# Kernel optimization log

Hardware: AMD Instinct MI355X
Metric: run time of the kernel (lower is better)

The kernel has to match this reference:

```python
import jax, jax.numpy as jnp
import numpy as np

B, C, H, W = 4, 256, 256, 256
N_BOX = 64          # rois per batch element
S = 7               # roi_feature_size[0]
ROI_SCALE = 0.25    # world -> feature-map coordinate scale
WORLD = H / ROI_SCALE  # world extent ~1024


def setup_inputs() -> dict:
    key = jax.random.key(0)
    k1, k2, k3, k4 = jax.random.split(key, 4)
    feats = jax.random.normal(k1, (B, C, H, W), dtype=jnp.float32)
    centers = jax.random.uniform(k2, (B, N_BOX, 2), minval=0.0, maxval=WORLD)
    wh = jax.random.uniform(k3, (B, N_BOX, 2), minval=32.0, maxval=256.0)
    theta = jax.random.uniform(k4, (B, N_BOX, 1), minval=0.0, maxval=2.0 * np.pi)
    rois = jnp.concatenate([centers, wh, theta], axis=-1).astype(jnp.float32)  # [B,N,5]
    return {"feats": feats, "rois": rois}


def _rotated_roi_align(feats, rois, out_size):
    # feats: [B,C,H,W]; rois: [B,N,5] = (cx,cy,w,h,theta) in feature-map coords
    b, c, h, w = feats.shape
    n = rois.shape[1]
    feats_t = jnp.transpose(feats, (0, 2, 3, 1))            # [B,H,W,C]
    r = rois.reshape(b * n, 5)
    bidx = jnp.repeat(jnp.arange(b), n)                     # [BN]
    cx, cy, bw, bh, th = r[:, 0], r[:, 1], r[:, 2], r[:, 3], r[:, 4]
    # sample-point offsets in box-local coords (cell centers)
    lin = (jnp.arange(out_size, dtype=jnp.float32) + 0.5) / out_size - 0.5  # [S]
    u = lin[None, None, :] * bw[:, None, None]              # cols  [BN,1,S]
    v = lin[None, :, None] * bh[:, None, None]              # rows  [BN,S,1]
    ct, st = jnp.cos(th)[:, None, None], jnp.sin(th)[:, None, None]
    x = cx[:, None, None] + u * ct - v * st                 # [BN,S,S]
    y = cy[:, None, None] + u * st + v * ct                 # [BN,S,S]
    # bilinear sampling with zero padding outside the map
    x0 = jnp.floor(x); y0 = jnp.floor(y)
    x1 = x0 + 1.0;     y1 = y0 + 1.0
    wx1 = x - x0; wx0 = 1.0 - wx1
    wy1 = y - y0; wy0 = 1.0 - wy1

    def gather(xi, yi):
        valid = (xi >= 0) & (xi <= w - 1) & (yi >= 0) & (yi <= h - 1)
        xc = jnp.clip(xi, 0, w - 1).astype(jnp.int32)
        yc = jnp.clip(yi, 0, h - 1).astype(jnp.int32)
        vals = feats_t[bidx[:, None, None], yc, xc]          # [BN,S,S,C]
        return vals * valid[..., None].astype(feats.dtype)

    out = (gather(x0, y0) * (wx0 * wy0)[..., None]
           + gather(x1, y0) * (wx1 * wy0)[..., None]
           + gather(x0, y1) * (wx0 * wy1)[..., None]
           + gather(x1, y1) * (wx1 * wy1)[..., None])       # [BN,S,S,C]
    return jnp.transpose(out, (0, 3, 1, 2))                 # [BN,C,S,S]


def reference(feats, rois):
    # scale all roi entries except the trailing angle
    srois = jnp.concatenate([rois[..., :-1] * ROI_SCALE, rois[..., -1:]], axis=-1)
    return _rotated_roi_align(feats, srois, S)              # cat over batch -> [B*N,C,S,S]
```

## Files before the change

### kernel.cpp

```cpp
#include <hip/hip_runtime.h>

#define BB 4
#define CC 256
#define HH 256
#define WW 256
#define N_BOX 64
#define SS 7
#define NPTS (SS * SS)
#define NROI (BB * N_BOX)
#define CG 64
#define NG (CC / CG)
#define ITEMS (CG * NPTS)
#define ROI_SCALE 0.25f

__global__ __launch_bounds__(256) void rotated_roi_align_kernel(
    const float* __restrict__ feats,
    const float* __restrict__ rois,
    float* __restrict__ out)
{
    __shared__ int   s_off[4][NPTS];
    __shared__ float s_w[4][NPTS];

    const int r   = blockIdx.x;
    const int cq  = blockIdx.y;
    const int b   = r >> 6;
    const int tid = threadIdx.x;

    if (tid < NPTS) {
        const float cx = rois[r * 5 + 0] * ROI_SCALE;
        const float cy = rois[r * 5 + 1] * ROI_SCALE;
        const float bw = rois[r * 5 + 2] * ROI_SCALE;
        const float bh = rois[r * 5 + 3] * ROI_SCALE;
        const float th = rois[r * 5 + 4];
        const float ct = cosf(th);
        const float st = sinf(th);

        const int py = tid / SS;
        const int px = tid - py * SS;
        const float lu = (px + 0.5f) / (float)SS - 0.5f;
        const float lv = (py + 0.5f) / (float)SS - 0.5f;
        const float u = lu * bw;
        const float v = lv * bh;
        const float x = cx + u * ct - v * st;
        const float y = cy + u * st + v * ct;

        const float x0f = floorf(x), y0f = floorf(y);
        const float x1f = x0f + 1.0f, y1f = y0f + 1.0f;
        const float wx1 = x - x0f, wx0 = 1.0f - wx1;
        const float wy1 = y - y0f, wy0 = 1.0f - wy1;

        const bool vx0 = (x0f >= 0.0f) && (x0f <= (float)(WW - 1));
        const bool vx1 = (x1f >= 0.0f) && (x1f <= (float)(WW - 1));
        const bool vy0 = (y0f >= 0.0f) && (y0f <= (float)(HH - 1));
        const bool vy1 = (y1f >= 0.0f) && (y1f <= (float)(HH - 1));

        const int x0c = min(max((int)x0f, 0), WW - 1);
        const int x1c = min(max((int)x1f, 0), WW - 1);
        const int y0c = min(max((int)y0f, 0), HH - 1);
        const int y1c = min(max((int)y1f, 0), HH - 1);

        s_off[0][tid] = y0c * WW + x0c;  s_w[0][tid] = (vx0 && vy0) ? wx0 * wy0 : 0.0f;
        s_off[1][tid] = y0c * WW + x1c;  s_w[1][tid] = (vx1 && vy0) ? wx1 * wy0 : 0.0f;
        s_off[2][tid] = y1c * WW + x0c;  s_w[2][tid] = (vx0 && vy1) ? wx0 * wy1 : 0.0f;
        s_off[3][tid] = y1c * WW + x1c;  s_w[3][tid] = (vx1 && vy1) ? wx1 * wy1 : 0.0f;
    }
    __syncthreads();

    const float* plane_base = feats + ((size_t)b * CC + (size_t)cq * CG) * (HH * WW);
    float* ob = out + (size_t)r * CC * NPTS + (size_t)cq * CG * NPTS;

    #pragma unroll 4
    for (int i = tid; i < ITEMS; i += 256) {
        const int cl = i / NPTS;
        const int p  = i - cl * NPTS;
        const float* plane = plane_base + (size_t)cl * (HH * WW);
        const float v0 = plane[s_off[0][p]];
        const float v1 = plane[s_off[1][p]];
        const float v2 = plane[s_off[2][p]];
        const float v3 = plane[s_off[3][p]];
        ob[i] = s_w[0][p] * v0 + s_w[1][p] * v1 + s_w[2][p] * v2 + s_w[3][p] * v3;
    }
}

extern "C" void kernel_launch(void* const* d_in, const int* in_sizes, int n_in,
                              void* d_out, int out_size, void* d_ws, size_t ws_size,
                              hipStream_t stream) {
    const float* feats = (const float*)d_in[0];
    const float* rois  = (const float*)d_in[1];
    float* out = (float*)d_out;

    dim3 grid(NROI, NG);
    rotated_roi_align_kernel<<<grid, 256, 0, stream>>>(feats, rois, out);
}
```

Before: 401.9 us.

## Transpose features to channels-last in workspace before a coalesced float4 gather

Adds a tiled shared-memory transpose that converts the NCHW feature map into NHWC in the workspace buffer on every call. A new gather kernel then reads four contiguous channels per float4 load at each bilinear corner, accumulates the result, and transposes it back through shared memory into the [roi, C, S, S] output. This replaces the old pattern where every sample was a scattered 4-byte load from a different channel plane. The cost is a full read and write of the 268 MB feature tensor each call. If the workspace is too small, the code falls back to the original kernel.

```diff
diff --git a/kernel.cpp b/kernel.cpp
--- a/kernel.cpp
+++ b/kernel.cpp
@@ -4,28 +4,61 @@
 #define CC 256
 #define HH 256
 #define WW 256
+#define HWV (HH * WW)
 #define N_BOX 64
 #define SS 7
 #define NPTS (SS * SS)
 #define NROI (BB * N_BOX)
-#define CG 64
-#define NG (CC / CG)
-#define ITEMS (CG * NPTS)
 #define ROI_SCALE 0.25f
 
-__global__ __launch_bounds__(256) void rotated_roi_align_kernel(
-    const float* __restrict__ feats,
-    const float* __restrict__ rois,
+__global__ __launch_bounds__(256) void transpose_kernel(
+    const float* __restrict__ in,
     float* __restrict__ out)
 {
-    __shared__ int   s_off[4][NPTS];
-    __shared__ float s_w[4][NPTS];
-
-    const int r   = blockIdx.x;
-    const int cq  = blockIdx.y;
-    const int b   = r >> 6;
+    __shared__ float tile[64 * 65];
+
+    const int hw0 = blockIdx.x * 64;
+    const int c0  = blockIdx.y * 64;
+    const int b   = blockIdx.z;
     const int tid = threadIdx.x;
 
+    {
+        const int jq = tid & 15;
+        const int ir = tid >> 4;
+        const float* inb = in + ((size_t)(b * CC + c0) << 16) + hw0;
+        #pragma unroll
+        for (int k = 0; k < 4; ++k) {
+            const int i = ir + 16 * k;
+            const float4 v = *(const float4*)(inb + ((size_t)i << 16) + jq * 4);
+            tile[(jq * 4 + 0) * 65 + i] = v.x;
+            tile[(jq * 4 + 1) * 65 + i] = v.y;
+            tile[(jq * 4 + 2) * 65 + i] = v.z;
+            tile[(jq * 4 + 3) * 65 + i] = v.w;
+        }
+    }
+    __syncthreads();
+
+    {
+        const int iq = tid & 15;
+        const int jr = tid >> 4;
+        float* outb = out + (((size_t)b << 16) + hw0) * CC + c0;
+        #pragma unroll
+        for (int k = 0; k < 4; ++k) {
+            const int j = jr + 16 * k;
+            float4 v;
+            v.x = tile[j * 65 + iq * 4 + 0];
+            v.y = tile[j * 65 + iq * 4 + 1];
+            v.z = tile[j * 65 + iq * 4 + 2];
+            v.w = tile[j * 65 + iq * 4 + 3];
+            *(float4*)(outb + (size_t)j * CC + iq * 4) = v;
+        }
+    }
+}
+
+__device__ __forceinline__ void precompute_points(
+    const float* __restrict__ rois, int r, int tid,
+    int s_off[4][NPTS], float s_w[4][NPTS])
+{
     if (tid < NPTS) {
         const float cx = rois[r * 5 + 0] * ROI_SCALE;
         const float cy = rois[r * 5 + 1] * ROI_SCALE;
@@ -64,16 +97,83 @@
         s_off[2][tid] = y1c * WW + x0c;  s_w[2][tid] = (vx0 && vy1) ? wx0 * wy1 : 0.0f;
         s_off[3][tid] = y1c * WW + x1c;  s_w[3][tid] = (vx1 && vy1) ? wx1 * wy1 : 0.0f;
     }
-    __syncthreads();
-
-    const float* plane_base = feats + ((size_t)b * CC + (size_t)cq * CG) * (HH * WW);
-    float* ob = out + (size_t)r * CC * NPTS + (size_t)cq * CG * NPTS;
+}
+
+#define CGP 64
+#define NG2 (CC / CGP)
+#define TSTRIDE 65
+
+__global__ __launch_bounds__(256) void gather_cl_kernel(
+    const float* __restrict__ ft,
+    const float* __restrict__ rois,
+    float* __restrict__ out)
+{
+    __shared__ int   s_off[4][NPTS];
+    __shared__ float s_w[4][NPTS];
+    __shared__ float t[NPTS * TSTRIDE];
+
+    const int r   = blockIdx.x;
+    const int cg  = blockIdx.y;
+    const int b   = r >> 6;
+    const int tid = threadIdx.x;
+
+    precompute_points(rois, r, tid, s_off, s_w);
+    __syncthreads();
+
+    const float* base = ft + ((size_t)b << 16) * CC + cg * CGP;
+
+    for (int w = tid; w < NPTS * (CGP / 4); w += 256) {
+        const int p  = w >> 4;
+        const int cq = w & 15;
+        float4 acc = make_float4(0.f, 0.f, 0.f, 0.f);
+        #pragma unroll
+        for (int k = 0; k < 4; ++k) {
+            const float4 v = *(const float4*)(base + (size_t)s_off[k][p] * CC + cq * 4);
+            const float wk = s_w[k][p];
+            acc.x += wk * v.x;
+            acc.y += wk * v.y;
+            acc.z += wk * v.z;
+            acc.w += wk * v.w;
+        }
+        t[p * TSTRIDE + cq * 4 + 0] = acc.x;
+        t[p * TSTRIDE + cq * 4 + 1] = acc.y;
+        t[p * TSTRIDE + cq * 4 + 2] = acc.z;
+        t[p * TSTRIDE + cq * 4 + 3] = acc.w;
+    }
+    __syncthreads();
+
+    float* ob = out + ((size_t)r * CC + (size_t)cg * CGP) * NPTS;
+    for (int j = tid; j < CGP * NPTS; j += 256) {
+        const int c = j / NPTS;
+        const int p = j - c * NPTS;
+        ob[j] = t[p * TSTRIDE + c];
+    }
+}
+
+__global__ __launch_bounds__(256) void rotated_roi_align_fallback(
+    const float* __restrict__ feats,
+    const float* __restrict__ rois,
+    float* __restrict__ out)
+{
+    __shared__ int   s_off[4][NPTS];
+    __shared__ float s_w[4][NPTS];
+
+    const int r   = blockIdx.x;
+    const int cq  = blockIdx.y;
+    const int b   = r >> 6;
+    const int tid = threadIdx.x;
+
+    precompute_points(rois, r, tid, s_off, s_w);
+    __syncthreads();
+
+    const float* plane_base = feats + ((size_t)b * CC + (size_t)cq * 64) * HWV;
+    float* ob = out + (size_t)r * CC * NPTS + (size_t)cq * 64 * NPTS;
 
     #pragma unroll 4
-    for (int i = tid; i < ITEMS; i += 256) {
+    for (int i = tid; i < 64 * NPTS; i += 256) {
         const int cl = i / NPTS;
         const int p  = i - cl * NPTS;
-        const float* plane = plane_base + (size_t)cl * (HH * WW);
+        const float* plane = plane_base + (size_t)cl * HWV;
         const float v0 = plane[s_off[0][p]];
         const float v1 = plane[s_off[1][p]];
         const float v2 = plane[s_off[2][p]];
@@ -89,6 +189,16 @@
     const float* rois  = (const float*)d_in[1];
     float* out = (float*)d_out;
 
-    dim3 grid(NROI, NG);
-    rotated_roi_align_kernel<<<grid, 256, 0, stream>>>(feats, rois, out);
-}
+    const size_t need = (size_t)BB * CC * HWV * sizeof(float);
+
+    if (ws_size >= need) {
+        float* feats_t = (float*)d_ws;
+        dim3 g1(HWV / 64, CC / 64, BB);
+        transpose_kernel<<<g1, 256, 0, stream>>>(feats, feats_t);
+        dim3 g2(NROI, NG2);
+        gather_cl_kernel<<<g2, 256, 0, stream>>>(feats_t, rois, out);
+    } else {
+        dim3 grid(NROI, 4);
+        rotated_roi_align_fallback<<<grid, 256, 0, stream>>>(feats, rois, out);
+    }
+}
```

Measured after the change: 411.7 us. +2.4%, slower.

## Split ROI coordinate precompute into separate kernel and halve channel group size

Applied to the files above, without the earlier changes.

Moves the per-ROI sample-offset and weight computation (including sin/cos) into a small precompute kernel that writes to workspace, so each gather block only loads the 196 offsets and weights instead of recomputing them. Channel groups shrink from 64 to 32, doubling the grid to spread the scattered loads over more blocks, and the gather loop is restructured with a fixed trip count plus tail and a higher occupancy hint. The cost is an extra kernel launch and a round trip through global memory for the precomputed tables.

```diff
diff --git a/kernel.cpp b/kernel.cpp
--- a/kernel.cpp
+++ b/kernel.cpp
@@ -4,81 +4,114 @@
 #define CC 256
 #define HH 256
 #define WW 256
+#define HWV (HH * WW)
 #define N_BOX 64
 #define SS 7
 #define NPTS (SS * SS)
 #define NROI (BB * N_BOX)
-#define CG 64
-#define NG (CC / CG)
-#define ITEMS (CG * NPTS)
 #define ROI_SCALE 0.25f
 
-__global__ __launch_bounds__(256) void rotated_roi_align_kernel(
+#define CG 32
+#define NGRP (CC / CG)
+#define ITEMS (CG * NPTS)
+#define PPR (4 * NPTS)
+
+__global__ __launch_bounds__(64) void precompute_kernel(
+    const float* __restrict__ rois,
+    int* __restrict__ offs,
+    float* __restrict__ wts)
+{
+    const int r = blockIdx.x;
+    const int tid = threadIdx.x;
+    if (tid >= NPTS) return;
+
+    const float cx = rois[r * 5 + 0] * ROI_SCALE;
+    const float cy = rois[r * 5 + 1] * ROI_SCALE;
+    const float bw = rois[r * 5 + 2] * ROI_SCALE;
+    const float bh = rois[r * 5 + 3] * ROI_SCALE;
+    const float th = rois[r * 5 + 4];
+    const float ct = cosf(th);
+    const float st = sinf(th);
+
+    const int py = tid / SS;
+    const int px = tid - py * SS;
+    const float lu = (px + 0.5f) / (float)SS - 0.5f;
+    const float lv = (py + 0.5f) / (float)SS - 0.5f;
+    const float u = lu * bw;
+    const float v = lv * bh;
+    const float x = cx + u * ct - v * st;
+    const float y = cy + u * st + v * ct;
+
+    const float x0f = floorf(x), y0f = floorf(y);
+    const float x1f = x0f + 1.0f, y1f = y0f + 1.0f;
+    const float wx1 = x - x0f, wx0 = 1.0f - wx1;
+    const float wy1 = y - y0f, wy0 = 1.0f - wy1;
+
+    const bool vx0 = (x0f >= 0.0f) && (x0f <= (float)(WW - 1));
+    const bool vx1 = (x1f >= 0.0f) && (x1f <= (float)(WW - 1));
+    const bool vy0 = (y0f >= 0.0f) && (y0f <= (float)(HH - 1));
+    const bool vy1 = (y1f >= 0.0f) && (y1f <= (float)(HH - 1));
+
+    const int x0c = min(max((int)x0f, 0), WW - 1);
+    const int x1c = min(max((int)x1f, 0), WW - 1);
+    const int y0c = min(max((int)y0f, 0), HH - 1);
+    const int y1c = min(max((int)y1f, 0), HH - 1);
+
+    int*   ro = offs + (size_t)r * PPR;
+    float* rw = wts  + (size_t)r * PPR;
+    ro[0 * NPTS + tid] = y0c * WW + x0c;  rw[0 * NPTS + tid] = (vx0 && vy0) ? wx0 * wy0 : 0.0f;
+    ro[1 * NPTS + tid] = y0c * WW + x1c;  rw[1 * NPTS + tid] = (vx1 && vy0) ? wx1 * wy0 : 0.0f;
+    ro[2 * NPTS + tid] = y1c * WW + x0c;  rw[2 * NPTS + tid] = (vx0 && vy1) ? wx0 * wy1 : 0.0f;
+    ro[3 * NPTS + tid] = y1c * WW + x1c;  rw[3 * NPTS + tid] = (vx1 && vy1) ? wx1 * wy1 : 0.0f;
+}
+
+__global__ __launch_bounds__(256, 8) void gather_kernel(
     const float* __restrict__ feats,
-    const float* __restrict__ rois,
+    const int* __restrict__ offs,
+    const float* __restrict__ wts,
     float* __restrict__ out)
 {
-    __shared__ int   s_off[4][NPTS];
-    __shared__ float s_w[4][NPTS];
+    __shared__ int   s_off[PPR];
+    __shared__ float s_w[PPR];
 
     const int r   = blockIdx.x;
-    const int cq  = blockIdx.y;
+    const int cg  = blockIdx.y;
     const int b   = r >> 6;
     const int tid = threadIdx.x;
 
-    if (tid < NPTS) {
-        const float cx = rois[r * 5 + 0] * ROI_SCALE;
-        const float cy = rois[r * 5 + 1] * ROI_SCALE;
-        const float bw = rois[r * 5 + 2] * ROI_SCALE;
-        const float bh = rois[r * 5 + 3] * ROI_SCALE;
-        const float th = rois[r * 5 + 4];
-        const float ct = cosf(th);
-        const float st = sinf(th);
-
-        const int py = tid / SS;
-        const int px = tid - py * SS;
-        const float lu = (px + 0.5f) / (float)SS - 0.5f;
-        const float lv = (py + 0.5f) / (float)SS - 0.5f;
-        const float u = lu * bw;
-        const float v = lv * bh;
-        const float x = cx + u * ct - v * st;
-        const float y = cy + u * st + v * ct;
-
-        const float x0f = floorf(x), y0f = floorf(y);
-        const float x1f = x0f + 1.0f, y1f = y0f + 1.0f;
-        const float wx1 = x - x0f, wx0 = 1.0f - wx1;
-        const float wy1 = y - y0f, wy0 = 1.0f - wy1;
-
-        const bool vx0 = (x0f >= 0.0f) && (x0f <= (float)(WW - 1));
-        const bool vx1 = (x1f >= 0.0f) && (x1f <= (float)(WW - 1));
-        const bool vy0 = (y0f >= 0.0f) && (y0f <= (float)(HH - 1));
-        const bool vy1 = (y1f >= 0.0f) && (y1f <= (float)(HH - 1));
-
-        const int x0c = min(max((int)x0f, 0), WW - 1);
-        const int x1c = min(max((int)x1f, 0), WW - 1);
-        const int y0c = min(max((int)y0f, 0), HH - 1);
-        const int y1c = min(max((int)y1f, 0), HH - 1);
-
-        s_off[0][tid] = y0c * WW + x0c;  s_w[0][tid] = (vx0 && vy0) ? wx0 * wy0 : 0.0f;
-        s_off[1][tid] = y0c * WW + x1c;  s_w[1][tid] = (vx1 && vy0) ? wx1 * wy0 : 0.0f;
-        s_off[2][tid] = y1c * WW + x0c;  s_w[2][tid] = (vx0 && vy1) ? wx0 * wy1 : 0.0f;
-        s_off[3][tid] = y1c * WW + x1c;  s_w[3][tid] = (vx1 && vy1) ? wx1 * wy1 : 0.0f;
+    if (tid < PPR) {
+        s_off[tid] = offs[(size_t)r * PPR + tid];
+        s_w[tid]   = wts [(size_t)r * PPR + tid];
     }
     __syncthreads();
 
-    const float* plane_base = feats + ((size_t)b * CC + (size_t)cq * CG) * (HH * WW);
-    float* ob = out + (size_t)r * CC * NPTS + (size_t)cq * CG * NPTS;
+    const float* plane_base = feats + ((size_t)b * CC + (size_t)cg * CG) * HWV;
+    float* ob = out + ((size_t)r * CC + (size_t)cg * CG) * NPTS;
 
-    #pragma unroll 4
-    for (int i = tid; i < ITEMS; i += 256) {
+    #pragma unroll 3
+    for (int it = 0; it < 6; ++it) {
+        const int i  = tid + it * 256;
         const int cl = i / NPTS;
         const int p  = i - cl * NPTS;
-        const float* plane = plane_base + (size_t)cl * (HH * WW);
-        const float v0 = plane[s_off[0][p]];
-        const float v1 = plane[s_off[1][p]];
-        const float v2 = plane[s_off[2][p]];
-        const float v3 = plane[s_off[3][p]];
-        ob[i] = s_w[0][p] * v0 + s_w[1][p] * v1 + s_w[2][p] * v2 + s_w[3][p] * v3;
+        const float* plane = plane_base + (size_t)cl * HWV;
+        const float v0 = plane[s_off[0 * NPTS + p]];
+        const float v1 = plane[s_off[1 * NPTS + p]];
+        const float v2 = plane[s_off[2 * NPTS + p]];
+        const float v3 = plane[s_off[3 * NPTS + p]];
+        ob[i] = s_w[0 * NPTS + p] * v0 + s_w[1 * NPTS + p] * v1
+              + s_w[2 * NPTS + p] * v2 + s_w[3 * NPTS + p] * v3;
+    }
+    if (tid < ITEMS - 6 * 256) {
+        const int i  = tid + 6 * 256;
+        const int cl = i / NPTS;
+        const int p  = i - cl * NPTS;
+        const float* plane = plane_base + (size_t)cl * HWV;
+        const float v0 = plane[s_off[0 * NPTS + p]];
+        const float v1 = plane[s_off[1 * NPTS + p]];
+        const float v2 = plane[s_off[2 * NPTS + p]];
+        const float v3 = plane[s_off[3 * NPTS + p]];
+        ob[i] = s_w[0 * NPTS + p] * v0 + s_w[1 * NPTS + p] * v1
+              + s_w[2 * NPTS + p] * v2 + s_w[3 * NPTS + p] * v3;
     }
 }
 
@@ -89,6 +122,11 @@
     const float* rois  = (const float*)d_in[1];
     float* out = (float*)d_out;
 
-    dim3 grid(NROI, NG);
-    rotated_roi_align_kernel<<<grid, 256, 0, stream>>>(feats, rois, out);
+    int*   offs = (int*)d_ws;
+    float* wts  = (float*)((char*)d_ws + (size_t)NROI * PPR * sizeof(int));
+
+    precompute_kernel<<<NROI, 64, 0, stream>>>(rois, offs, wts);
+
+    dim3 g(NROI, NGRP);
+    gather_kernel<<<g, 256, 0, stream>>>(feats, offs, wts, out);
 }
```

After: 416.0 us. 3.5% more time.

## Precompute deduplicated float4 quad addresses and gather via shared memory

Applied to the files above, without the earlier changes.

Adds a precompute kernel that computes bilinear weights and deduplicates 16-byte-aligned quad addresses per ROI, storing slot indices in workspace. The gather kernel then loads each unique float4 quad once per channel into shared memory and combines the four taps from there, with 32 channels per block. This aims to cut redundant scattered global loads, but it serializes channels with two barriers per iteration, adds a second launch, and leaves most threads idle during combination.

```diff
diff --git a/kernel.cpp b/kernel.cpp
--- a/kernel.cpp
+++ b/kernel.cpp
@@ -4,26 +4,38 @@
 #define CC 256
 #define HH 256
 #define WW 256
+#define HWV (HH * WW)
 #define N_BOX 64
 #define SS 7
 #define NPTS (SS * SS)
 #define NROI (BB * N_BOX)
-#define CG 64
-#define NG (CC / CG)
-#define ITEMS (CG * NPTS)
 #define ROI_SCALE 0.25f
 
-__global__ __launch_bounds__(256) void rotated_roi_align_kernel(
-    const float* __restrict__ feats,
+#define NCAND (NPTS * 4)
+#define CG 32
+#define NGRP (CC / CG)
+
+#define WS_WTS_OFF   0
+#define WS_SLOT_OFF  (WS_WTS_OFF + NROI * NPTS * 16)
+#define WS_UOFF_OFF  (WS_SLOT_OFF + NROI * NPTS * 8)
+#define WS_APK_OFF   (WS_UOFF_OFF + NROI * NCAND * 4)
+#define WS_NU_OFF    (WS_APK_OFF + NROI * NPTS * 4)
+#define WS_NEED      (WS_NU_OFF + NROI * 4)
+
+__global__ __launch_bounds__(256) void precompute_kernel(
     const float* __restrict__ rois,
-    float* __restrict__ out)
+    float4* __restrict__ g_wts,
+    short4* __restrict__ g_slots,
+    int* __restrict__ g_uoff,
+    int* __restrict__ g_apk,
+    int* __restrict__ g_nu)
 {
-    __shared__ int   s_off[4][NPTS];
-    __shared__ float s_w[4][NPTS];
-
-    const int r   = blockIdx.x;
-    const int cq  = blockIdx.y;
-    const int b   = r >> 6;
+    __shared__ int cand[NCAND];
+    __shared__ int lead[NCAND];
+    __shared__ int flag[NCAND];
+    __shared__ int pre[NCAND];
+
+    const int r = blockIdx.x;
     const int tid = threadIdx.x;
 
     if (tid < NPTS) {
@@ -59,6 +71,151 @@
         const int y0c = min(max((int)y0f, 0), HH - 1);
         const int y1c = min(max((int)y1f, 0), HH - 1);
 
+        const int q0 = x0c & ~3;
+        const int q1 = x1c & ~3;
+        cand[tid * 4 + 0] = (y0c << 8) + q0;
+        cand[tid * 4 + 1] = (y0c << 8) + q1;
+        cand[tid * 4 + 2] = (y1c << 8) + q0;
+        cand[tid * 4 + 3] = (y1c << 8) + q1;
+
+        float4 w;
+        w.x = (vx0 && vy0) ? wx0 * wy0 : 0.0f;
+        w.y = (vx1 && vy0) ? wx1 * wy0 : 0.0f;
+        w.z = (vx0 && vy1) ? wx0 * wy1 : 0.0f;
+        w.w = (vx1 && vy1) ? wx1 * wy1 : 0.0f;
+        g_wts[(size_t)r * NPTS + tid] = w;
+        g_apk[(size_t)r * NPTS + tid] = (x0c & 3) | ((x1c & 3) << 2);
+    }
+    __syncthreads();
+
+    if (tid < NCAND) {
+        const int c = cand[tid];
+        int ld = tid;
+        for (int j = 0; j < NCAND; ++j) {
+            const int cj = cand[j];
+            if (j < tid && cj == c && ld == tid) ld = j;
+        }
+        lead[tid] = ld;
+        flag[tid] = (ld == tid) ? 1 : 0;
+    }
+    __syncthreads();
+
+    if (tid < NCAND) {
+        int s = 0;
+        for (int j = 0; j < NCAND; ++j) {
+            const int f = flag[j];
+            if (j < tid) s += f;
+        }
+        pre[tid] = s;
+        if (flag[tid]) g_uoff[(size_t)r * NCAND + s] = cand[tid];
+    }
+    __syncthreads();
+
+    if (tid < NPTS) {
+        short4 sl;
+        sl.x = (short)pre[lead[tid * 4 + 0]];
+        sl.y = (short)pre[lead[tid * 4 + 1]];
+        sl.z = (short)pre[lead[tid * 4 + 2]];
+        sl.w = (short)pre[lead[tid * 4 + 3]];
+        g_slots[(size_t)r * NPTS + tid] = sl;
+    }
+    if (tid == 0) g_nu[r] = pre[NCAND - 1] + flag[NCAND - 1];
+}
+
+__global__ __launch_bounds__(256, 8) void gather_kernel(
+    const float* __restrict__ feats,
+    const float4* __restrict__ g_wts,
+    const short4* __restrict__ g_slots,
+    const int* __restrict__ g_uoff,
+    const int* __restrict__ g_apk,
+    const int* __restrict__ g_nu,
+    float* __restrict__ out)
+{
+    __shared__ int    s_uoff[NCAND];
+    __shared__ short4 s_slot[NPTS];
+    __shared__ int    s_apk[NPTS];
+    __shared__ float4 s_wts[NPTS];
+    __shared__ float4 s_quad[NCAND];
+    __shared__ float  s_out[CG * NPTS];
+
+    const int r   = blockIdx.x;
+    const int cg  = blockIdx.y;
+    const int b   = r >> 6;
+    const int tid = threadIdx.x;
+
+    const int nu = g_nu[r];
+    if (tid < NCAND && tid < nu) s_uoff[tid] = g_uoff[(size_t)r * NCAND + tid];
+    if (tid < NPTS) {
+        s_slot[tid] = g_slots[(size_t)r * NPTS + tid];
+        s_apk[tid]  = g_apk[(size_t)r * NPTS + tid];
+        s_wts[tid]  = g_wts[(size_t)r * NPTS + tid];
+    }
+    __syncthreads();
+
+    const float* gbase = feats + (((size_t)b * CC + (size_t)cg * CG) << 16);
+
+    for (int cl = 0; cl < CG; ++cl) {
+        const float* plane = gbase + ((size_t)cl << 16);
+        if (tid < nu) s_quad[tid] = *(const float4*)(plane + s_uoff[tid]);
+        __syncthreads();
+        if (tid < NPTS) {
+            const short4 sl = s_slot[tid];
+            const int ap = s_apk[tid];
+            const int a0 = ap & 3;
+            const int a1 = (ap >> 2) & 3;
+            const float4 w = s_wts[tid];
+            const float v00 = ((const float*)&s_quad[sl.x])[a0];
+            const float v01 = ((const float*)&s_quad[sl.y])[a1];
+            const float v10 = ((const float*)&s_quad[sl.z])[a0];
+            const float v11 = ((const float*)&s_quad[sl.w])[a1];
+            s_out[cl * NPTS + tid] = w.x * v00 + w.y * v01 + w.z * v10 + w.w * v11;
+        }
+        __syncthreads();
+    }
+
+    float* ob = out + (((size_t)r * CC + (size_t)cg * CG) * NPTS);
+    for (int j = tid; j < CG * NPTS; j += 256) ob[j] = s_out[j];
+}
+
+__global__ __launch_bounds__(256) void fallback_kernel(
+    const float* __restrict__ feats,
+    const float* __restrict__ rois,
+    float* __restrict__ out)
+{
+    __shared__ int   s_off[4][NPTS];
+    __shared__ float s_w[4][NPTS];
+
+    const int r   = blockIdx.x;
+    const int cq  = blockIdx.y;
+    const int b   = r >> 6;
+    const int tid = threadIdx.x;
+
+    if (tid < NPTS) {
+        const float cx = rois[r * 5 + 0] * ROI_SCALE;
+        const float cy = rois[r * 5 + 1] * ROI_SCALE;
+        const float bw = rois[r * 5 + 2] * ROI_SCALE;
+        const float bh = rois[r * 5 + 3] * ROI_SCALE;
+        const float th = rois[r * 5 + 4];
+        const float ct = cosf(th), st = sinf(th);
+        const int py = tid / SS;
+        const int px = tid - py * SS;
+        const float lu = (px + 0.5f) / (float)SS - 0.5f;
+        const float lv = (py + 0.5f) / (float)SS - 0.5f;
+        const float u = lu * bw, v = lv * bh;
+        const float x = cx + u * ct - v * st;
+        const float y = cy + u * st + v * ct;
+        const float x0f = floorf(x), y0f = floorf(y);
+        const float x1f = x0f + 1.0f, y1f = y0f + 1.0f;
+        const float wx1 = x - x0f, wx0 = 1.0f - wx1;
+        const float wy1 = y - y0f, wy0 = 1.0f - wy1;
+        const bool vx0 = (x0f >= 0.0f) && (x0f <= (float)(WW - 1));
+        const bool vx1 = (x1f >= 0.0f) && (x1f <= (float)(WW - 1));
+        const bool vy0 = (y0f >= 0.0f) && (y0f <= (float)(HH - 1));
+        const bool vy1 = (y1f >= 0.0f) && (y1f <= (float)(HH - 1));
+        const int x0c = min(max((int)x0f, 0), WW - 1);
+        const int x1c = min(max((int)x1f, 0), WW - 1);
+        const int y0c = min(max((int)y0f, 0), HH - 1);
+        const int y1c = min(max((int)y1f, 0), HH - 1);
         s_off[0][tid] = y0c * WW + x0c;  s_w[0][tid] = (vx0 && vy0) ? wx0 * wy0 : 0.0f;
         s_off[1][tid] = y0c * WW + x1c;  s_w[1][tid] = (vx1 && vy0) ? wx1 * wy0 : 0.0f;
         s_off[2][tid] = y1c * WW + x0c;  s_w[2][tid] = (vx0 && vy1) ? wx0 * wy1 : 0.0f;
@@ -66,19 +223,16 @@
     }
     __syncthreads();
 
-    const float* plane_base = feats + ((size_t)b * CC + (size_t)cq * CG) * (HH * WW);
-    float* ob = out + (size_t)r * CC * NPTS + (size_t)cq * CG * NPTS;
+    const float* plane_base = feats + ((size_t)b * CC + (size_t)cq * 64) * HWV;
+    float* ob = out + (size_t)r * CC * NPTS + (size_t)cq * 64 * NPTS;
 
     #pragma unroll 4
-    for (int i = tid; i < ITEMS; i += 256) {
+    for (int i = tid; i < 64 * NPTS; i += 256) {
         const int cl = i / NPTS;
         const int p  = i - cl * NPTS;
-        const float* plane = plane_base + (size_t)cl * (HH * WW);
-        const float v0 = plane[s_off[0][p]];
-        const float v1 = plane[s_off[1][p]];
-        const float v2 = plane[s_off[2][p]];
-        const float v3 = plane[s_off[3][p]];
-        ob[i] = s_w[0][p] * v0 + s_w[1][p] * v1 + s_w[2][p] * v2 + s_w[3][p] * v3;
+        const float* plane = plane_base + (size_t)cl * HWV;
+        ob[i] = s_w[0][p] * plane[s_off[0][p]] + s_w[1][p] * plane[s_off[1][p]]
+              + s_w[2][p] * plane[s_off[2][p]] + s_w[3][p] * plane[s_off[3][p]];
     }
 }
 
@@ -89,6 +243,21 @@
     const float* rois  = (const float*)d_in[1];
     float* out = (float*)d_out;
 
-    dim3 grid(NROI, NG);
-    rotated_roi_align_kernel<<<grid, 256, 0, stream>>>(feats, rois, out);
-}
+    if (ws_size < (size_t)WS_NEED) {
+        dim3 grid(NROI, 4);
+        fallback_kernel<<<grid, 256, 0, stream>>>(feats, rois, out);
+        return;
+    }
+
+    char* ws = (char*)d_ws;
+    float4* g_wts   = (float4*)(ws + WS_WTS_OFF);
+    short4* g_slots = (short4*)(ws + WS_SLOT_OFF);
+    int*    g_uoff  = (int*)(ws + WS_UOFF_OFF);
+    int*    g_apk   = (int*)(ws + WS_APK_OFF);
+    int*    g_nu    = (int*)(ws + WS_NU_OFF);
+
+    precompute_kernel<<<NROI, 256, 0, stream>>>(rois, g_wts, g_slots, g_uoff, g_apk, g_nu);
+
+    dim3 g(NROI, NGRP);
+    gather_kernel<<<g, 256, 0, stream>>>(feats, g_wts, g_slots, g_uoff, g_apk, g_nu, out);
+}
```

Result: no change. 408.3 us (+1.6%).
